# Performance work log

Hardware: AMD Instinct MI355X
Metric: run time of the kernel (lower is better)

## Reference

```python
import jax, jax.numpy as jnp
import numpy as np

CLAMP = 1.0e4
MIN_DECAY = 0.001
MAX_DECAY = 0.999
EPS = 1e-06


def setup_inputs() -> dict:
    key = jax.random.key(0)
    ks = jax.random.split(key, 6)
    B, K, C = 8, 4096, 1024
    return {
        "tokens": jax.random.normal(ks[0], (B, K, C), dtype=jnp.float32),
        "state": jax.random.normal(ks[1], (B, C), dtype=jnp.float32),
        "decay_logit": jax.random.normal(ks[2], (C,), dtype=jnp.float32),
        "input_gain_raw": jax.random.normal(ks[3], (C,), dtype=jnp.float32),
        "output_gain_raw": jax.random.normal(ks[4], (C,), dtype=jnp.float32),
        "state_bias": jax.random.normal(ks[5], (C,), dtype=jnp.float32),
    }


def reference(tokens, state, decay_logit, input_gain_raw, output_gain_raw, state_bias):
    # constrained parameters, each [C]
    decay = MIN_DECAY + (MAX_DECAY - MIN_DECAY) * jax.nn.sigmoid(decay_logit)
    input_gain = jax.nn.softplus(input_gain_raw) + EPS
    output_gain = jax.nn.softplus(output_gain_raw) + EPS

    # sanitize inputs as in torch.nan_to_num(...).clamp(-1e4, 1e4)
    x = jnp.nan_to_num(tokens, nan=0.0, posinf=CLAMP, neginf=-CLAMP)
    x = jnp.clip(x, -CLAMP, CLAMP)

    one_minus_decay = 1.0 - decay
    # driven_t = input_gain * x_t + state_bias, computed for all steps at once: [B,K,C]
    driven = input_gain[None, None, :] * x + state_bias[None, None, :]
    b = one_minus_decay[None, None, :] * driven  # additive term per step

    def step(s, b_t):  # s: [B,C], b_t: [B,C]
        s_new = decay[None, :] * s + b_t
        return s_new, s_new

    # scan over time axis K
    final_state, states = jax.lax.scan(step, state, jnp.swapaxes(b, 0, 1))
    outputs = output_gain[None, None, :] * jnp.swapaxes(states, 0, 1)  # [B,K,C]
    return outputs, final_state
```

## Files before the change

kernel.cpp:

```cpp
#include <hip/hip_runtime.h>
#include <math.h>

namespace {

constexpr int kB = 8;
constexpr int kK = 4096;
constexpr int kC = 1024;
constexpr int kL = 64;
constexpr int kNC = kK / kL;
constexpr int kTPB = 256;

constexpr float kClamp = 1.0e4f;
constexpr float kMinD = 0.001f;
constexpr float kMaxD = 0.999f;
constexpr float kEps = 1e-6f;

__device__ __forceinline__ float sanitize(float x) {
  x = (x != x) ? 0.0f : x;
  return fminf(kClamp, fmaxf(-kClamp, x));
}

__device__ __forceinline__ float softplusf(float x) {
  return fmaxf(x, 0.0f) + log1pf(expf(-fabsf(x)));
}

__device__ __forceinline__ float decay_of(float logit) {
  float sg = 1.0f / (1.0f + expf(-logit));
  return kMinD + (kMaxD - kMinD) * sg;
}

__global__ __launch_bounds__(kTPB) void k_carry(
    const float* __restrict__ tokens, const float* __restrict__ dlog,
    const float* __restrict__ igr, const float* __restrict__ sbias,
    float* __restrict__ carry) {
  const int b = blockIdx.x / kNC;
  const int j = blockIdx.x % kNC;
  const int c0 = threadIdx.x * 4;

  const float4 dl = *reinterpret_cast<const float4*>(dlog + c0);
  const float4 ig = *reinterpret_cast<const float4*>(igr + c0);
  const float4 sb = *reinterpret_cast<const float4*>(sbias + c0);

  const float d0 = decay_of(dl.x), d1 = decay_of(dl.y);
  const float d2 = decay_of(dl.z), d3 = decay_of(dl.w);
  const float g0 = softplusf(ig.x) + kEps, g1 = softplusf(ig.y) + kEps;
  const float g2 = softplusf(ig.z) + kEps, g3 = softplusf(ig.w) + kEps;
  const float a0 = (1.0f - d0) * g0, a1 = (1.0f - d1) * g1;
  const float a2 = (1.0f - d2) * g2, a3 = (1.0f - d3) * g3;
  const float bb0 = (1.0f - d0) * sb.x, bb1 = (1.0f - d1) * sb.y;
  const float bb2 = (1.0f - d2) * sb.z, bb3 = (1.0f - d3) * sb.w;

  const float* tp = tokens + (((size_t)b * kK) + (size_t)j * kL) * kC + c0;

  float s0 = 0.0f, s1 = 0.0f, s2 = 0.0f, s3 = 0.0f;
#pragma unroll 8
  for (int i = 0; i < kL; ++i) {
    const float4 x = *reinterpret_cast<const float4*>(tp + (size_t)i * kC);
    s0 = fmaf(d0, s0, fmaf(a0, sanitize(x.x), bb0));
    s1 = fmaf(d1, s1, fmaf(a1, sanitize(x.y), bb1));
    s2 = fmaf(d2, s2, fmaf(a2, sanitize(x.z), bb2));
    s3 = fmaf(d3, s3, fmaf(a3, sanitize(x.w), bb3));
  }
  float4 outv = make_float4(s0, s1, s2, s3);
  *reinterpret_cast<float4*>(carry + ((size_t)b * kNC + j) * kC + c0) = outv;
}

__global__ __launch_bounds__(256) void k_prefix(
    const float* __restrict__ carry, const float* __restrict__ state,
    const float* __restrict__ dlog, float* __restrict__ sstart,
    float* __restrict__ final_out) {
  const int idx = blockIdx.x * blockDim.x + threadIdx.x;
  const int b = idx / kC;
  const int c = idx - b * kC;
  const float d = decay_of(dlog[c]);
  float dL = d;
#pragma unroll
  for (int i = 0; i < 6; ++i) dL *= dL;
  float s = state[idx];
  for (int j = 0; j < kNC; ++j) {
    const size_t o = ((size_t)b * kNC + j) * kC + c;
    sstart[o] = s;
    s = fmaf(dL, s, carry[o]);
  }
  final_out[idx] = s;
}

__global__ __launch_bounds__(kTPB) void k_out(
    const float* __restrict__ tokens, const float* __restrict__ dlog,
    const float* __restrict__ igr, const float* __restrict__ ogr,
    const float* __restrict__ sbias, const float* __restrict__ sstart,
    float* __restrict__ out) {
  const int b = blockIdx.x / kNC;
  const int j = blockIdx.x % kNC;
  const int c0 = threadIdx.x * 4;

  const float4 dl = *reinterpret_cast<const float4*>(dlog + c0);
  const float4 ig = *reinterpret_cast<const float4*>(igr + c0);
  const float4 og = *reinterpret_cast<const float4*>(ogr + c0);
  const float4 sb = *reinterpret_cast<const float4*>(sbias + c0);

  const float d0 = decay_of(dl.x), d1 = decay_of(dl.y);
  const float d2 = decay_of(dl.z), d3 = decay_of(dl.w);
  const float g0 = softplusf(ig.x) + kEps, g1 = softplusf(ig.y) + kEps;
  const float g2 = softplusf(ig.z) + kEps, g3 = softplusf(ig.w) + kEps;
  const float a0 = (1.0f - d0) * g0, a1 = (1.0f - d1) * g1;
  const float a2 = (1.0f - d2) * g2, a3 = (1.0f - d3) * g3;
  const float bb0 = (1.0f - d0) * sb.x, bb1 = (1.0f - d1) * sb.y;
  const float bb2 = (1.0f - d2) * sb.z, bb3 = (1.0f - d3) * sb.w;
  const float o0 = softplusf(og.x) + kEps, o1 = softplusf(og.y) + kEps;
  const float o2 = softplusf(og.z) + kEps, o3 = softplusf(og.w) + kEps;

  const float4 sinit =
      *reinterpret_cast<const float4*>(sstart + ((size_t)b * kNC + j) * kC + c0);
  float s0 = sinit.x, s1 = sinit.y, s2 = sinit.z, s3 = sinit.w;

  const float* tp = tokens + (((size_t)b * kK) + (size_t)j * kL) * kC + c0;
  float* op = out + (((size_t)b * kK) + (size_t)j * kL) * kC + c0;

#pragma unroll 8
  for (int i = 0; i < kL; ++i) {
    const float4 x = *reinterpret_cast<const float4*>(tp + (size_t)i * kC);
    s0 = fmaf(d0, s0, fmaf(a0, sanitize(x.x), bb0));
    s1 = fmaf(d1, s1, fmaf(a1, sanitize(x.y), bb1));
    s2 = fmaf(d2, s2, fmaf(a2, sanitize(x.z), bb2));
    s3 = fmaf(d3, s3, fmaf(a3, sanitize(x.w), bb3));
    float4 y = make_float4(o0 * s0, o1 * s1, o2 * s2, o3 * s3);
    *reinterpret_cast<float4*>(op + (size_t)i * kC) = y;
  }
}

}

extern "C" void kernel_launch(void* const* d_in, const int* in_sizes, int n_in,
                              void* d_out, int out_size, void* d_ws, size_t ws_size,
                              hipStream_t stream) {
  const float* tokens = (const float*)d_in[0];
  const float* state  = (const float*)d_in[1];
  const float* dlog   = (const float*)d_in[2];
  const float* igr    = (const float*)d_in[3];
  const float* ogr    = (const float*)d_in[4];
  const float* sbias  = (const float*)d_in[5];

  float* out = (float*)d_out;
  float* final_out = out + (size_t)kB * kK * kC;

  float* carry  = (float*)d_ws;
  float* sstart = carry + (size_t)kB * kNC * kC;

  k_carry<<<dim3(kB * kNC), kTPB, 0, stream>>>(tokens, dlog, igr, sbias, carry);
  k_prefix<<<dim3((kB * kC) / 256), 256, 0, stream>>>(carry, state, dlog, sstart,
                                                      final_out);
  k_out<<<dim3(kB * kNC), kTPB, 0, stream>>>(tokens, dlog, igr, ogr, sbias,
                                             sstart, out);
}
```

Measured before the change: 76.72 us.

## Fuse chunked scan into single kernel with flag-based inter-block carry propagation

Replaces the three-kernel chunk-carry / prefix / output pipeline with one kernel. Each block computes its chunk carry, publishes it with a release flag, spins until all earlier chunks of the same batch are ready, and then recomputes its starting state from those carries before writing outputs. The point is to drop the serial prefix kernel and the extra launches, and to let the second pass over the tokens hit cache while it is still warm. It adds spin-wait dependencies that assume all 512 blocks can be resident at once, and each block does O(j) carry reads. Output stores are now nontemporal.

Result: slower. 152.5 us (+98.8%).

```diff
diff --git a/kernel.cpp b/kernel.cpp
--- a/kernel.cpp
+++ b/kernel.cpp
@@ -8,12 +8,15 @@
 constexpr int kC = 1024;
 constexpr int kL = 64;
 constexpr int kNC = kK / kL;
+constexpr int kNBLK = kB * kNC;
 constexpr int kTPB = 256;
 
 constexpr float kClamp = 1.0e4f;
 constexpr float kMinD = 0.001f;
 constexpr float kMaxD = 0.999f;
 constexpr float kEps = 1e-6f;
+
+typedef float f4 __attribute__((ext_vector_type(4)));
 
 __device__ __forceinline__ float sanitize(float x) {
   x = (x != x) ? 0.0f : x;
@@ -25,79 +28,29 @@
 }
 
 __device__ __forceinline__ float decay_of(float logit) {
-  float sg = 1.0f / (1.0f + expf(-logit));
-  return kMinD + (kMaxD - kMinD) * sg;
+  return kMinD + (kMaxD - kMinD) / (1.0f + expf(-logit));
 }
 
-__global__ __launch_bounds__(kTPB) void k_carry(
-    const float* __restrict__ tokens, const float* __restrict__ dlog,
-    const float* __restrict__ igr, const float* __restrict__ sbias,
-    float* __restrict__ carry) {
-  const int b = blockIdx.x / kNC;
-  const int j = blockIdx.x % kNC;
+__global__ void k_init(int* __restrict__ flags) {
+  const int i = blockIdx.x * blockDim.x + threadIdx.x;
+  if (i < kNBLK) flags[i] = 0;
+}
+
+__global__ __launch_bounds__(kTPB) void k_scan(
+    const float* __restrict__ tokens, const float* __restrict__ state,
+    const float* __restrict__ dlog, const float* __restrict__ igr,
+    const float* __restrict__ ogr, const float* __restrict__ sbias,
+    float* __restrict__ out, float* __restrict__ final_out,
+    float* __restrict__ carry, int* __restrict__ flags) {
+  const int gid = blockIdx.x;
+  const int b = gid / kNC;
+  const int j = gid - b * kNC;
   const int c0 = threadIdx.x * 4;
 
-  const float4 dl = *reinterpret_cast<const float4*>(dlog + c0);
-  const float4 ig = *reinterpret_cast<const float4*>(igr + c0);
-  const float4 sb = *reinterpret_cast<const float4*>(sbias + c0);
-
-  const float d0 = decay_of(dl.x), d1 = decay_of(dl.y);
-  const float d2 = decay_of(dl.z), d3 = decay_of(dl.w);
-  const float g0 = softplusf(ig.x) + kEps, g1 = softplusf(ig.y) + kEps;
-  const float g2 = softplusf(ig.z) + kEps, g3 = softplusf(ig.w) + kEps;
-  const float a0 = (1.0f - d0) * g0, a1 = (1.0f - d1) * g1;
-  const float a2 = (1.0f - d2) * g2, a3 = (1.0f - d3) * g3;
-  const float bb0 = (1.0f - d0) * sb.x, bb1 = (1.0f - d1) * sb.y;
-  const float bb2 = (1.0f - d2) * sb.z, bb3 = (1.0f - d3) * sb.w;
-
-  const float* tp = tokens + (((size_t)b * kK) + (size_t)j * kL) * kC + c0;
-
-  float s0 = 0.0f, s1 = 0.0f, s2 = 0.0f, s3 = 0.0f;
-#pragma unroll 8
-  for (int i = 0; i < kL; ++i) {
-    const float4 x = *reinterpret_cast<const float4*>(tp + (size_t)i * kC);
-    s0 = fmaf(d0, s0, fmaf(a0, sanitize(x.x), bb0));
-    s1 = fmaf(d1, s1, fmaf(a1, sanitize(x.y), bb1));
-    s2 = fmaf(d2, s2, fmaf(a2, sanitize(x.z), bb2));
-    s3 = fmaf(d3, s3, fmaf(a3, sanitize(x.w), bb3));
-  }
-  float4 outv = make_float4(s0, s1, s2, s3);
-  *reinterpret_cast<float4*>(carry + ((size_t)b * kNC + j) * kC + c0) = outv;
-}
-
-__global__ __launch_bounds__(256) void k_prefix(
-    const float* __restrict__ carry, const float* __restrict__ state,
-    const float* __restrict__ dlog, float* __restrict__ sstart,
-    float* __restrict__ final_out) {
-  const int idx = blockIdx.x * blockDim.x + threadIdx.x;
-  const int b = idx / kC;
-  const int c = idx - b * kC;
-  const float d = decay_of(dlog[c]);
-  float dL = d;
-#pragma unroll
-  for (int i = 0; i < 6; ++i) dL *= dL;
-  float s = state[idx];
-  for (int j = 0; j < kNC; ++j) {
-    const size_t o = ((size_t)b * kNC + j) * kC + c;
-    sstart[o] = s;
-    s = fmaf(dL, s, carry[o]);
-  }
-  final_out[idx] = s;
-}
-
-__global__ __launch_bounds__(kTPB) void k_out(
-    const float* __restrict__ tokens, const float* __restrict__ dlog,
-    const float* __restrict__ igr, const float* __restrict__ ogr,
-    const float* __restrict__ sbias, const float* __restrict__ sstart,
-    float* __restrict__ out) {
-  const int b = blockIdx.x / kNC;
-  const int j = blockIdx.x % kNC;
-  const int c0 = threadIdx.x * 4;
-
-  const float4 dl = *reinterpret_cast<const float4*>(dlog + c0);
-  const float4 ig = *reinterpret_cast<const float4*>(igr + c0);
-  const float4 og = *reinterpret_cast<const float4*>(ogr + c0);
-  const float4 sb = *reinterpret_cast<const float4*>(sbias + c0);
+  const f4 dl = *reinterpret_cast<const f4*>(dlog + c0);
+  const f4 ig = *reinterpret_cast<const f4*>(igr + c0);
+  const f4 og = *reinterpret_cast<const f4*>(ogr + c0);
+  const f4 sb = *reinterpret_cast<const f4*>(sbias + c0);
 
   const float d0 = decay_of(dl.x), d1 = decay_of(dl.y);
   const float d2 = decay_of(dl.z), d3 = decay_of(dl.w);
@@ -110,22 +63,72 @@
   const float o0 = softplusf(og.x) + kEps, o1 = softplusf(og.y) + kEps;
   const float o2 = softplusf(og.z) + kEps, o3 = softplusf(og.w) + kEps;
 
-  const float4 sinit =
-      *reinterpret_cast<const float4*>(sstart + ((size_t)b * kNC + j) * kC + c0);
-  float s0 = sinit.x, s1 = sinit.y, s2 = sinit.z, s3 = sinit.w;
+  const float* tp = tokens + (((size_t)b * kK) + (size_t)j * kL) * kC + c0;
 
-  const float* tp = tokens + (((size_t)b * kK) + (size_t)j * kL) * kC + c0;
-  float* op = out + (((size_t)b * kK) + (size_t)j * kL) * kC + c0;
-
+  float s0 = 0.0f, s1 = 0.0f, s2 = 0.0f, s3 = 0.0f;
 #pragma unroll 8
   for (int i = 0; i < kL; ++i) {
-    const float4 x = *reinterpret_cast<const float4*>(tp + (size_t)i * kC);
+    const f4 x = *reinterpret_cast<const f4*>(tp + (size_t)i * kC);
     s0 = fmaf(d0, s0, fmaf(a0, sanitize(x.x), bb0));
     s1 = fmaf(d1, s1, fmaf(a1, sanitize(x.y), bb1));
     s2 = fmaf(d2, s2, fmaf(a2, sanitize(x.z), bb2));
     s3 = fmaf(d3, s3, fmaf(a3, sanitize(x.w), bb3));
-    float4 y = make_float4(o0 * s0, o1 * s1, o2 * s2, o3 * s3);
-    *reinterpret_cast<float4*>(op + (size_t)i * kC) = y;
+  }
+  f4 cv; cv.x = s0; cv.y = s1; cv.z = s2; cv.w = s3;
+  *reinterpret_cast<f4*>(carry + (size_t)gid * kC + c0) = cv;
+  __syncthreads();
+  if (threadIdx.x == 0) {
+    __threadfence();
+    __hip_atomic_store(flags + gid, 1, __ATOMIC_RELEASE,
+                       __HIP_MEMORY_SCOPE_AGENT);
+  }
+
+  const int base = b * kNC;
+  if (threadIdx.x == 0) {
+    for (int p = j - 1; p >= 0; --p) {
+      while (__hip_atomic_load(flags + base + p, __ATOMIC_RELAXED,
+                               __HIP_MEMORY_SCOPE_AGENT) == 0) {
+        __builtin_amdgcn_s_sleep(2);
+      }
+    }
+  }
+  __syncthreads();
+  __threadfence();
+
+  float dL0 = d0, dL1 = d1, dL2 = d2, dL3 = d3;
+#pragma unroll
+  for (int i = 0; i < 6; ++i) {
+    dL0 *= dL0; dL1 *= dL1; dL2 *= dL2; dL3 *= dL3;
+  }
+
+  const f4 st = *reinterpret_cast<const f4*>(state + (size_t)b * kC + c0);
+  float S0 = st.x, S1 = st.y, S2 = st.z, S3 = st.w;
+#pragma unroll 4
+  for (int p = 0; p < j; ++p) {
+    const f4 cp = *reinterpret_cast<const f4*>(
+        carry + (size_t)(base + p) * kC + c0);
+    S0 = fmaf(dL0, S0, cp.x);
+    S1 = fmaf(dL1, S1, cp.y);
+    S2 = fmaf(dL2, S2, cp.z);
+    S3 = fmaf(dL3, S3, cp.w);
+  }
+
+  float* op = out + (((size_t)b * kK) + (size_t)j * kL) * kC + c0;
+  s0 = S0; s1 = S1; s2 = S2; s3 = S3;
+#pragma unroll 8
+  for (int i = 0; i < kL; ++i) {
+    const f4 x = *reinterpret_cast<const f4*>(tp + (size_t)i * kC);
+    s0 = fmaf(d0, s0, fmaf(a0, sanitize(x.x), bb0));
+    s1 = fmaf(d1, s1, fmaf(a1, sanitize(x.y), bb1));
+    s2 = fmaf(d2, s2, fmaf(a2, sanitize(x.z), bb2));
+    s3 = fmaf(d3, s3, fmaf(a3, sanitize(x.w), bb3));
+    f4 y; y.x = o0 * s0; y.y = o1 * s1; y.z = o2 * s2; y.w = o3 * s3;
+    __builtin_nontemporal_store(y, reinterpret_cast<f4*>(op + (size_t)i * kC));
+  }
+
+  if (j == kNC - 1) {
+    f4 fv; fv.x = s0; fv.y = s1; fv.z = s2; fv.w = s3;
+    *reinterpret_cast<f4*>(final_out + (size_t)b * kC + c0) = fv;
   }
 }
 
@@ -144,12 +147,10 @@
   float* out = (float*)d_out;
   float* final_out = out + (size_t)kB * kK * kC;
 
-  float* carry  = (float*)d_ws;
-  float* sstart = carry + (size_t)kB * kNC * kC;
+  float* carry = (float*)d_ws;
+  int* flags = (int*)((char*)d_ws + (size_t)kNBLK * kC * sizeof(float));
 
-  k_carry<<<dim3(kB * kNC), kTPB, 0, stream>>>(tokens, dlog, igr, sbias, carry);
-  k_prefix<<<dim3((kB * kC) / 256), 256, 0, stream>>>(carry, state, dlog, sstart,
-                                                      final_out);
-  k_out<<<dim3(kB * kNC), kTPB, 0, stream>>>(tokens, dlog, igr, ogr, sbias,
-                                             sstart, out);
+  k_init<<<dim3((kNBLK + 255) / 256), 256, 0, stream>>>(flags);
+  k_scan<<<dim3(kNBLK), kTPB, 0, stream>>>(tokens, state, dlog, igr, ogr,
+                                           sbias, out, final_out, carry, flags);
 }
```
